# Kernel optimization log

Hardware: AMD Instinct MI355X
Metric: run time of the kernel (lower is better)

Reference implementation:

```python
import jax, jax.numpy as jnp
import numpy as np

N_NODES = 100000
N_EDGES = 1600000
K_HOPS = 10


def setup_inputs() -> dict:
    key = jax.random.key(0)
    ks = jax.random.split(key, 8)
    x = jax.random.normal(ks[0], (N_NODES, 512), dtype=jnp.float32)
    edge_src = jax.random.randint(ks[1], (N_EDGES,), 0, N_NODES, dtype=jnp.int32)
    edge_dst = jax.random.randint(ks[2], (N_EDGES,), 0, N_NODES, dtype=jnp.int32)
    # positive, roughly degree-normalized edge weights (stand-in for sym-normalized adj)
    edge_weight = jax.random.uniform(ks[3], (N_EDGES,), dtype=jnp.float32) / 16.0
    node_index = jax.random.randint(ks[4], (10000,), 0, N_NODES, dtype=jnp.int32)
    W1 = jax.random.normal(ks[5], (512, 64), dtype=jnp.float32) * 0.05
    W2 = jax.random.normal(ks[6], (64, 64), dtype=jnp.float32) * 0.05
    w_prop = jax.random.normal(ks[7], (64, 1), dtype=jnp.float32) * 0.05
    return {"x": x, "edge_src": edge_src, "edge_dst": edge_dst,
            "edge_weight": edge_weight, "node_index": node_index,
            "W1": W1, "W2": W2, "w_prop": w_prop}


def reference(x, edge_src, edge_dst, edge_weight, node_index, W1, W2, w_prop):
    # MLP (dropout is identity at inference, use_bias=False)
    h = jax.nn.relu(x @ W1)          # [N, 64]
    h = jax.nn.relu(h @ W2)          # [N, C]

    # K-hop sparse propagation: h_{k+1} = A @ h_k via edge-list SpMM
    def spmm(v):
        return jax.ops.segment_sum(edge_weight[:, None] * v[edge_src],
                                   edge_dst, num_segments=N_NODES)

    props = [h]
    cur = h
    for _ in range(K_HOPS):
        cur = spmm(cur)
        props.append(cur)
    H = jnp.stack(props, axis=1)     # [N, K+1, C]

    # sigmoid-gated combination across hops (DAGNN)
    score = jax.nn.sigmoid(H @ w_prop)        # [N, K+1, 1]
    out = jnp.sum(score * H, axis=1)          # [N, C]

    # gather requested nodes
    return out[node_index]                    # [n_idx, C]
```

## Files before the change

### kernel.cpp

```cpp
#include <hip/hip_runtime.h>
#include <hip/hip_bf16.h>

#define C 64

__device__ __forceinline__ float b2f(unsigned short s) {
    return __uint_as_float(((unsigned int)s) << 16);
}
__device__ __forceinline__ unsigned short f2b(float f) {
    unsigned int u = __float_as_uint(f);
    u = (u + 0x7FFF + ((u >> 16) & 1)) >> 16;
    return (unsigned short)u;
}

__launch_bounds__(256)
__global__ void mlp_kernel(const float* __restrict__ x,
                           const float* __restrict__ W1,
                           const float* __restrict__ W2,
                           float* __restrict__ h0,
                           unsigned short* __restrict__ hb, int nN)
{
    __shared__ float smem[5440];
    float (*As)[36] = (float(*)[36])smem;
    float (*Bs)[68] = (float(*)[68])(smem + 2304);
    float (*Hs)[68] = (float(*)[68])smem;
    float (*Ws)[68] = (float(*)[68])(smem + 4352);

    const int t  = threadIdx.x;
    const int ty = t >> 4;
    const int tx = t & 15;
    const int row0 = blockIdx.x * 64;

    float acc[4][4] = {};

    for (int k0 = 0; k0 < 512; k0 += 32) {
        #pragma unroll
        for (int h = 0; h < 2; ++h) {
            int f = t + 256 * h;
            int r  = f >> 3;
            int lk = (f & 7) * 4;
            int grow = row0 + r;
            float4 v = make_float4(0.f, 0.f, 0.f, 0.f);
            if (grow < nN) v = *(const float4*)&x[(size_t)grow * 512 + k0 + lk];
            *(float4*)&As[r][lk] = v;
        }
        #pragma unroll
        for (int h = 0; h < 2; ++h) {
            int f = t + 256 * h;
            int kr = f >> 4;
            int c4 = (f & 15) * 4;
            *(float4*)&Bs[kr][c4] = *(const float4*)&W1[(size_t)(k0 + kr) * 64 + c4];
        }
        __syncthreads();

        for (int kk = 0; kk < 32; kk += 4) {
            float4 b0 = *(float4*)&Bs[kk + 0][tx * 4];
            float4 b1 = *(float4*)&Bs[kk + 1][tx * 4];
            float4 b2 = *(float4*)&Bs[kk + 2][tx * 4];
            float4 b3 = *(float4*)&Bs[kk + 3][tx * 4];
            #pragma unroll
            for (int i = 0; i < 4; ++i) {
                float4 a = *(float4*)&As[ty * 4 + i][kk];
                acc[i][0] += a.x * b0.x + a.y * b1.x + a.z * b2.x + a.w * b3.x;
                acc[i][1] += a.x * b0.y + a.y * b1.y + a.z * b2.y + a.w * b3.y;
                acc[i][2] += a.x * b0.z + a.y * b1.z + a.z * b2.z + a.w * b3.z;
                acc[i][3] += a.x * b0.w + a.y * b1.w + a.z * b2.w + a.w * b3.w;
            }
        }
        __syncthreads();
    }

    #pragma unroll
    for (int i = 0; i < 4; ++i) {
        float4 o;
        o.x = acc[i][0] > 0.f ? acc[i][0] : 0.f;
        o.y = acc[i][1] > 0.f ? acc[i][1] : 0.f;
        o.z = acc[i][2] > 0.f ? acc[i][2] : 0.f;
        o.w = acc[i][3] > 0.f ? acc[i][3] : 0.f;
        *(float4*)&Hs[ty * 4 + i][tx * 4] = o;
    }

    float acc2[4][4] = {};
    for (int k0w = 0; k0w < 64; k0w += 16) {
        __syncthreads();
        {
            int r  = t >> 4;
            int c4 = (t & 15) * 4;
            *(float4*)&Ws[r][c4] = *(const float4*)&W2[(size_t)(k0w + r) * 64 + c4];
        }
        __syncthreads();

        for (int kk = 0; kk < 16; kk += 4) {
            float4 b0 = *(float4*)&Ws[kk + 0][tx * 4];
            float4 b1 = *(float4*)&Ws[kk + 1][tx * 4];
            float4 b2 = *(float4*)&Ws[kk + 2][tx * 4];
            float4 b3 = *(float4*)&Ws[kk + 3][tx * 4];
            #pragma unroll
            for (int i = 0; i < 4; ++i) {
                float4 a = *(float4*)&Hs[ty * 4 + i][k0w + kk];
                acc2[i][0] += a.x * b0.x + a.y * b1.x + a.z * b2.x + a.w * b3.x;
                acc2[i][1] += a.x * b0.y + a.y * b1.y + a.z * b2.y + a.w * b3.y;
                acc2[i][2] += a.x * b0.z + a.y * b1.z + a.z * b2.z + a.w * b3.z;
                acc2[i][3] += a.x * b0.w + a.y * b1.w + a.z * b2.w + a.w * b3.w;
            }
        }
    }

    #pragma unroll
    for (int i = 0; i < 4; ++i) {
        int grow = row0 + ty * 4 + i;
        if (grow < nN) {
            float4 o;
            o.x = acc2[i][0] > 0.f ? acc2[i][0] : 0.f;
            o.y = acc2[i][1] > 0.f ? acc2[i][1] : 0.f;
            o.z = acc2[i][2] > 0.f ? acc2[i][2] : 0.f;
            o.w = acc2[i][3] > 0.f ? acc2[i][3] : 0.f;
            *(float4*)&h0[(size_t)grow * 64 + tx * 4] = o;
            ushort4 ob = make_ushort4(f2b(o.x), f2b(o.y), f2b(o.z), f2b(o.w));
            *(ushort4*)&hb[(size_t)grow * 64 + tx * 4] = ob;
        }
    }
}

__launch_bounds__(256)
__global__ void count_kernel(const int* __restrict__ dst, int* __restrict__ rowptr, int nE)
{
    int e = blockIdx.x * 256 + threadIdx.x;
    if (e < nE) atomicAdd(&rowptr[dst[e]], 1);
}

__launch_bounds__(256)
__global__ void scanA(int* __restrict__ deg, int* __restrict__ bsum, int nN)
{
    __shared__ int ts[256];
    const int t = threadIdx.x;
    const int base = blockIdx.x * 1024 + t * 4;
    int v0 = 0, v1 = 0, v2 = 0, v3 = 0;
    if (base + 3 < nN) {
        int4 v = *(const int4*)&deg[base];
        v0 = v.x; v1 = v.y; v2 = v.z; v3 = v.w;
    } else {
        if (base + 0 < nN) v0 = deg[base + 0];
        if (base + 1 < nN) v1 = deg[base + 1];
        if (base + 2 < nN) v2 = deg[base + 2];
        if (base + 3 < nN) v3 = deg[base + 3];
    }
    int s = v0 + v1 + v2 + v3;
    ts[t] = s;
    __syncthreads();
    for (int d = 1; d < 256; d <<= 1) {
        int xv = (t >= d) ? ts[t - d] : 0;
        __syncthreads();
        ts[t] += xv;
        __syncthreads();
    }
    if (t == 255) bsum[blockIdx.x] = ts[255];
    int e0 = ts[t] - s;
    int e1 = e0 + v0;
    int e2 = e1 + v1;
    int e3 = e2 + v2;
    if (base + 3 < nN) {
        *(int4*)&deg[base] = make_int4(e0, e1, e2, e3);
    } else {
        if (base + 0 < nN) deg[base + 0] = e0;
        if (base + 1 < nN) deg[base + 1] = e1;
        if (base + 2 < nN) deg[base + 2] = e2;
        if (base + 3 < nN) deg[base + 3] = e3;
    }
}

__launch_bounds__(256)
__global__ void scanB(int* __restrict__ bsum, int nB)
{
    __shared__ int ts[256];
    const int t = threadIdx.x;
    int v = (t < nB) ? bsum[t] : 0;
    ts[t] = v;
    __syncthreads();
    for (int d = 1; d < 256; d <<= 1) {
        int xv = (t >= d) ? ts[t - d] : 0;
        __syncthreads();
        ts[t] += xv;
        __syncthreads();
    }
    if (t < nB) bsum[t] = ts[t] - v;
}

__launch_bounds__(256)
__global__ void scanC(int* __restrict__ deg, const int* __restrict__ bsum, int nN)
{
    const int i4 = (blockIdx.x * 256 + threadIdx.x) * 4;
    if (i4 >= nN) return;
    const int b = bsum[i4 >> 10];
    if (i4 + 3 < nN) {
        int4 v = *(int4*)&deg[i4];
        v.x += b; v.y += b; v.z += b; v.w += b;
        *(int4*)&deg[i4] = v;
    } else {
        for (int j = 0; j < 4 && i4 + j < nN; ++j) deg[i4 + j] += b;
    }
}

__launch_bounds__(256)
__global__ void fill_kernel(const int* __restrict__ src, const int* __restrict__ dst,
                            const float* __restrict__ w,
                            int* __restrict__ rowptr,
                            int2* __restrict__ cwp, int nE)
{
    int e = blockIdx.x * 256 + threadIdx.x;
    if (e >= nE) return;
    int d = dst[e];
    int pos = atomicAdd(&rowptr[d], 1);
    cwp[pos] = make_int2(src[e], __float_as_int(w[e]));
}

__launch_bounds__(256)
__global__ void spmm_fused(const int* __restrict__ rowptr,
                           const int2* __restrict__ cwp,
                           const unsigned short* __restrict__ cur,
                           unsigned short* __restrict__ nxt,
                           const int* __restrict__ idx,
                           const float* __restrict__ wp,
                           float* __restrict__ out,
                           int nN, int nI, int nodeBlocks)
{
    const int bid  = blockIdx.x;
    const int wid  = threadIdx.x >> 6;
    const int lane = threadIdx.x & 63;
    const int g = lane >> 3;
    const int q = lane & 7;

    int node, oi = -1;
    if (bid < nodeBlocks) {
        node = bid * 4 + wid;
        if (node >= nN) return;
    } else {
        oi = (bid - nodeBlocks) * 4 + wid;
        if (oi >= nI) return;
        node = idx[oi];
    }

    const int beg = (node == 0) ? 0 : rowptr[node - 1];
    const int end = rowptr[node];

    float a0[8] = {}, a1[8] = {};

    for (int e = beg; e < end; e += 16) {
        int ea = e + g;
        int eb = ea + 8;
        int2 ca = (ea < end) ? cwp[ea] : make_int2(0, 0);
        int2 cb = (eb < end) ? cwp[eb] : make_int2(0, 0);
        float wa = __int_as_float(ca.y);
        float wb = __int_as_float(cb.y);
        int4 ra = *(const int4*)&cur[(size_t)ca.x * 64 + q * 8];
        int4 rb = *(const int4*)&cur[(size_t)cb.x * 64 + q * 8];
        a0[0] += wa * __uint_as_float((unsigned)ra.x << 16);
        a0[1] += wa * __uint_as_float((unsigned)ra.x & 0xFFFF0000u);
        a0[2] += wa * __uint_as_float((unsigned)ra.y << 16);
        a0[3] += wa * __uint_as_float((unsigned)ra.y & 0xFFFF0000u);
        a0[4] += wa * __uint_as_float((unsigned)ra.z << 16);
        a0[5] += wa * __uint_as_float((unsigned)ra.z & 0xFFFF0000u);
        a0[6] += wa * __uint_as_float((unsigned)ra.w << 16);
        a0[7] += wa * __uint_as_float((unsigned)ra.w & 0xFFFF0000u);
        a1[0] += wb * __uint_as_float((unsigned)rb.x << 16);
        a1[1] += wb * __uint_as_float((unsigned)rb.x & 0xFFFF0000u);
        a1[2] += wb * __uint_as_float((unsigned)rb.y << 16);
        a1[3] += wb * __uint_as_float((unsigned)rb.y & 0xFFFF0000u);
        a1[4] += wb * __uint_as_float((unsigned)rb.z << 16);
        a1[5] += wb * __uint_as_float((unsigned)rb.z & 0xFFFF0000u);
        a1[6] += wb * __uint_as_float((unsigned)rb.w << 16);
        a1[7] += wb * __uint_as_float((unsigned)rb.w & 0xFFFF0000u);
    }
    #pragma unroll
    for (int j = 0; j < 8; ++j) a0[j] += a1[j];

    #pragma unroll
    for (int j = 0; j < 8; ++j) {
        a0[j] += __shfl_xor(a0[j], 8);
        a0[j] += __shfl_xor(a0[j], 16);
        a0[j] += __shfl_xor(a0[j], 32);
    }

    if (oi < 0) {
        if (g == 0) {
            int4 ob;
            ob.x = (int)(((unsigned)f2b(a0[1]) << 16) | (unsigned)f2b(a0[0]));
            ob.y = (int)(((unsigned)f2b(a0[3]) << 16) | (unsigned)f2b(a0[2]));
            ob.z = (int)(((unsigned)f2b(a0[5]) << 16) | (unsigned)f2b(a0[4]));
            ob.w = (int)(((unsigned)f2b(a0[7]) << 16) | (unsigned)f2b(a0[6]));
            *(int4*)&nxt[(size_t)node * 64 + q * 8] = ob;
        }
    } else {
        float s = 0.f;
        #pragma unroll
        for (int j = 0; j < 8; ++j) s += a0[j] * wp[q * 8 + j];
        s += __shfl_xor(s, 1); s += __shfl_xor(s, 2); s += __shfl_xor(s, 4);
        float gate = 1.f / (1.f + __expf(-s));
        if (g == 0) {
            float* op = &out[(size_t)oi * 64 + q * 8];
            float4 p0 = *(float4*)op;
            float4 p1 = *(float4*)(op + 4);
            p0.x += gate * a0[0]; p0.y += gate * a0[1];
            p0.z += gate * a0[2]; p0.w += gate * a0[3];
            p1.x += gate * a0[4]; p1.y += gate * a0[5];
            p1.z += gate * a0[6]; p1.w += gate * a0[7];
            *(float4*)op = p0;
            *(float4*)(op + 4) = p1;
        }
    }
}

__launch_bounds__(256)
__global__ void gate_gather(const float* __restrict__ h,
                            const int* __restrict__ idx,
                            const float* __restrict__ wp,
                            float* __restrict__ out, int nI)
{
    int gid = blockIdx.x * 256 + threadIdx.x;
    int i = gid >> 6;
    if (i >= nI) return;
    int c = gid & 63;
    int n = idx[i];
    float v = h[(size_t)n * 64 + c];
    float s = v * wp[c];
    #pragma unroll
    for (int off = 32; off > 0; off >>= 1)
        s += __shfl_xor(s, off);
    float gate = 1.f / (1.f + __expf(-s));
    out[gid] = gate * v;
}

extern "C" void kernel_launch(void* const* d_in, const int* in_sizes, int n_in,
                              void* d_out, int out_size, void* d_ws, size_t ws_size,
                              hipStream_t stream) {
    const float* x    = (const float*)d_in[0];
    const int*   esrc = (const int*)d_in[1];
    const int*   edst = (const int*)d_in[2];
    const float* ew   = (const float*)d_in[3];
    const int*   nidx = (const int*)d_in[4];
    const float* W1   = (const float*)d_in[5];
    const float* W2   = (const float*)d_in[6];
    const float* wp   = (const float*)d_in[7];
    float* out = (float*)d_out;

    const int nN = in_sizes[0] / 512;
    const int nE = in_sizes[1];
    const int nI = in_sizes[4];

    float*          h0     = (float*)d_ws;
    unsigned short* bufA   = (unsigned short*)(h0 + (size_t)nN * C);
    unsigned short* bufB   = bufA + (size_t)nN * C;
    int*            rowptr = (int*)(bufB + (size_t)nN * C);
    int2*           cwp    = (int2*)(rowptr + nN);
    int*            bsum   = (int*)bufB;

    const int nB = (nN + 1023) / 1024;

    hipMemsetAsync(rowptr, 0, (size_t)nN * sizeof(int), stream);
    count_kernel<<<(nE + 255) / 256, 256, 0, stream>>>(edst, rowptr, nE);
    scanA<<<nB, 256, 0, stream>>>(rowptr, bsum, nN);
    scanB<<<1, 256, 0, stream>>>(bsum, nB);
    scanC<<<nB, 256, 0, stream>>>(rowptr, bsum, nN);
    fill_kernel<<<(nE + 255) / 256, 256, 0, stream>>>(esrc, edst, ew, rowptr, cwp, nE);

    mlp_kernel<<<(nN + 63) / 64, 256, 0, stream>>>(x, W1, W2, h0, bufA, nN);

    gate_gather<<<(nI * 64 + 255) / 256, 256, 0, stream>>>(h0, nidx, wp, out, nI);

    unsigned short* cur = bufA;
    unsigned short* nxt = bufB;
    const int nodeBlocks = (nN + 3) / 4;
    const int idxBlocks  = (nI + 3) / 4;
    for (int k = 0; k < 10; ++k) {
        const int nb = (k == 9) ? 0 : nodeBlocks;
        spmm_fused<<<nb + idxBlocks, 256, 0, stream>>>(
            rowptr, cwp, cur, nxt, nidx, wp, out, nN, nI, nb);
        unsigned short* tmp = cur; cur = nxt; nxt = tmp;
    }
}
```

Before: 1.192 ms.

## Split bf16 hop features into two 32-channel planes and widen MLP K-tile

Stores the bf16 propagation buffers as two separate 32-channel planes and launches separate block ranges per plane. Each wavefront gathers 64-byte half-rows for 16 edges at a time. The aim is to shrink each plane's working set so the random gathers hit cache better. The cost is reading the CSR edge list twice and launching twice as many node blocks. The MLP kernel also moves to a 64-wide K tile, loads W2 once with a single barrier, and uses more shared memory.

```diff
diff --git a/kernel.cpp b/kernel.cpp
--- a/kernel.cpp
+++ b/kernel.cpp
@@ -19,9 +19,9 @@
                            float* __restrict__ h0,
                            unsigned short* __restrict__ hb, int nN)
 {
-    __shared__ float smem[5440];
-    float (*As)[36] = (float(*)[36])smem;
-    float (*Bs)[68] = (float(*)[68])(smem + 2304);
+    __shared__ float smem[8704];
+    float (*As)[68] = (float(*)[68])smem;
+    float (*Bs)[68] = (float(*)[68])(smem + 4352);
     float (*Hs)[68] = (float(*)[68])smem;
     float (*Ws)[68] = (float(*)[68])(smem + 4352);
 
@@ -30,29 +30,28 @@
     const int tx = t & 15;
     const int row0 = blockIdx.x * 64;
 
+    const int srow = t >> 4;
+    const int slk  = (t & 15) * 4;
+
     float acc[4][4] = {};
 
-    for (int k0 = 0; k0 < 512; k0 += 32) {
-        #pragma unroll
-        for (int h = 0; h < 2; ++h) {
-            int f = t + 256 * h;
-            int r  = f >> 3;
-            int lk = (f & 7) * 4;
+    for (int k0 = 0; k0 < 512; k0 += 64) {
+        #pragma unroll
+        for (int h = 0; h < 4; ++h) {
+            int r = srow + 16 * h;
             int grow = row0 + r;
             float4 v = make_float4(0.f, 0.f, 0.f, 0.f);
-            if (grow < nN) v = *(const float4*)&x[(size_t)grow * 512 + k0 + lk];
-            *(float4*)&As[r][lk] = v;
-        }
-        #pragma unroll
-        for (int h = 0; h < 2; ++h) {
-            int f = t + 256 * h;
-            int kr = f >> 4;
-            int c4 = (f & 15) * 4;
-            *(float4*)&Bs[kr][c4] = *(const float4*)&W1[(size_t)(k0 + kr) * 64 + c4];
-        }
-        __syncthreads();
-
-        for (int kk = 0; kk < 32; kk += 4) {
+            if (grow < nN) v = *(const float4*)&x[(size_t)grow * 512 + k0 + slk];
+            *(float4*)&As[r][slk] = v;
+        }
+        #pragma unroll
+        for (int h = 0; h < 4; ++h) {
+            int r = srow + 16 * h;
+            *(float4*)&Bs[r][slk] = *(const float4*)&W1[(size_t)(k0 + r) * 64 + slk];
+        }
+        __syncthreads();
+
+        for (int kk = 0; kk < 64; kk += 4) {
             float4 b0 = *(float4*)&Bs[kk + 0][tx * 4];
             float4 b1 = *(float4*)&Bs[kk + 1][tx * 4];
             float4 b2 = *(float4*)&Bs[kk + 2][tx * 4];
@@ -78,33 +77,30 @@
         o.w = acc[i][3] > 0.f ? acc[i][3] : 0.f;
         *(float4*)&Hs[ty * 4 + i][tx * 4] = o;
     }
+    #pragma unroll
+    for (int qq = 0; qq < 4; ++qq) {
+        int r = srow + 16 * qq;
+        *(float4*)&Ws[r][slk] = *(const float4*)&W2[(size_t)r * 64 + slk];
+    }
+    __syncthreads();
 
     float acc2[4][4] = {};
-    for (int k0w = 0; k0w < 64; k0w += 16) {
-        __syncthreads();
-        {
-            int r  = t >> 4;
-            int c4 = (t & 15) * 4;
-            *(float4*)&Ws[r][c4] = *(const float4*)&W2[(size_t)(k0w + r) * 64 + c4];
-        }
-        __syncthreads();
-
-        for (int kk = 0; kk < 16; kk += 4) {
-            float4 b0 = *(float4*)&Ws[kk + 0][tx * 4];
-            float4 b1 = *(float4*)&Ws[kk + 1][tx * 4];
-            float4 b2 = *(float4*)&Ws[kk + 2][tx * 4];
-            float4 b3 = *(float4*)&Ws[kk + 3][tx * 4];
-            #pragma unroll
-            for (int i = 0; i < 4; ++i) {
-                float4 a = *(float4*)&Hs[ty * 4 + i][k0w + kk];
-                acc2[i][0] += a.x * b0.x + a.y * b1.x + a.z * b2.x + a.w * b3.x;
-                acc2[i][1] += a.x * b0.y + a.y * b1.y + a.z * b2.y + a.w * b3.y;
-                acc2[i][2] += a.x * b0.z + a.y * b1.z + a.z * b2.z + a.w * b3.z;
-                acc2[i][3] += a.x * b0.w + a.y * b1.w + a.z * b2.w + a.w * b3.w;
-            }
-        }
-    }
-
+    for (int kk = 0; kk < 64; kk += 4) {
+        float4 b0 = *(float4*)&Ws[kk + 0][tx * 4];
+        float4 b1 = *(float4*)&Ws[kk + 1][tx * 4];
+        float4 b2 = *(float4*)&Ws[kk + 2][tx * 4];
+        float4 b3 = *(float4*)&Ws[kk + 3][tx * 4];
+        #pragma unroll
+        for (int i = 0; i < 4; ++i) {
+            float4 a = *(float4*)&Hs[ty * 4 + i][kk];
+            acc2[i][0] += a.x * b0.x + a.y * b1.x + a.z * b2.x + a.w * b3.x;
+            acc2[i][1] += a.x * b0.y + a.y * b1.y + a.z * b2.y + a.w * b3.y;
+            acc2[i][2] += a.x * b0.z + a.y * b1.z + a.z * b2.z + a.w * b3.z;
+            acc2[i][3] += a.x * b0.w + a.y * b1.w + a.z * b2.w + a.w * b3.w;
+        }
+    }
+
+    const size_t planeStride = (size_t)nN * 32;
     #pragma unroll
     for (int i = 0; i < 4; ++i) {
         int grow = row0 + ty * 4 + i;
@@ -116,7 +112,8 @@
             o.w = acc2[i][3] > 0.f ? acc2[i][3] : 0.f;
             *(float4*)&h0[(size_t)grow * 64 + tx * 4] = o;
             ushort4 ob = make_ushort4(f2b(o.x), f2b(o.y), f2b(o.z), f2b(o.w));
-            *(ushort4*)&hb[(size_t)grow * 64 + tx * 4] = ob;
+            *(ushort4*)&hb[(size_t)(tx >> 3) * planeStride
+                           + (size_t)grow * 32 + (tx & 7) * 4] = ob;
         }
     }
 }
@@ -226,15 +223,15 @@
     const int bid  = blockIdx.x;
     const int wid  = threadIdx.x >> 6;
     const int lane = threadIdx.x & 63;
-    const int g = lane >> 3;
-    const int q = lane & 7;
-
-    int node, oi = -1;
-    if (bid < nodeBlocks) {
-        node = bid * 4 + wid;
+    const size_t planeStride = (size_t)nN * 32;
+
+    int node, oi = -1, plane = 0;
+    if (bid < 2 * nodeBlocks) {
+        plane = (bid >= nodeBlocks) ? 1 : 0;
+        node = (bid - plane * nodeBlocks) * 4 + wid;
         if (node >= nN) return;
     } else {
-        oi = (bid - nodeBlocks) * 4 + wid;
+        oi = (bid - 2 * nodeBlocks) * 4 + wid;
         if (oi >= nI) return;
         node = idx[oi];
     }
@@ -242,54 +239,82 @@
     const int beg = (node == 0) ? 0 : rowptr[node - 1];
     const int end = rowptr[node];
 
-    float a0[8] = {}, a1[8] = {};
-
-    for (int e = beg; e < end; e += 16) {
-        int ea = e + g;
-        int eb = ea + 8;
-        int2 ca = (ea < end) ? cwp[ea] : make_int2(0, 0);
-        int2 cb = (eb < end) ? cwp[eb] : make_int2(0, 0);
-        float wa = __int_as_float(ca.y);
-        float wb = __int_as_float(cb.y);
-        int4 ra = *(const int4*)&cur[(size_t)ca.x * 64 + q * 8];
-        int4 rb = *(const int4*)&cur[(size_t)cb.x * 64 + q * 8];
-        a0[0] += wa * __uint_as_float((unsigned)ra.x << 16);
-        a0[1] += wa * __uint_as_float((unsigned)ra.x & 0xFFFF0000u);
-        a0[2] += wa * __uint_as_float((unsigned)ra.y << 16);
-        a0[3] += wa * __uint_as_float((unsigned)ra.y & 0xFFFF0000u);
-        a0[4] += wa * __uint_as_float((unsigned)ra.z << 16);
-        a0[5] += wa * __uint_as_float((unsigned)ra.z & 0xFFFF0000u);
-        a0[6] += wa * __uint_as_float((unsigned)ra.w << 16);
-        a0[7] += wa * __uint_as_float((unsigned)ra.w & 0xFFFF0000u);
-        a1[0] += wb * __uint_as_float((unsigned)rb.x << 16);
-        a1[1] += wb * __uint_as_float((unsigned)rb.x & 0xFFFF0000u);
-        a1[2] += wb * __uint_as_float((unsigned)rb.y << 16);
-        a1[3] += wb * __uint_as_float((unsigned)rb.y & 0xFFFF0000u);
-        a1[4] += wb * __uint_as_float((unsigned)rb.z << 16);
-        a1[5] += wb * __uint_as_float((unsigned)rb.z & 0xFFFF0000u);
-        a1[6] += wb * __uint_as_float((unsigned)rb.w << 16);
-        a1[7] += wb * __uint_as_float((unsigned)rb.w & 0xFFFF0000u);
-    }
-    #pragma unroll
-    for (int j = 0; j < 8; ++j) a0[j] += a1[j];
-
-    #pragma unroll
-    for (int j = 0; j < 8; ++j) {
-        a0[j] += __shfl_xor(a0[j], 8);
-        a0[j] += __shfl_xor(a0[j], 16);
-        a0[j] += __shfl_xor(a0[j], 32);
-    }
-
     if (oi < 0) {
+        const int g  = lane >> 2;
+        const int q4 = lane & 3;
+        const unsigned short* curp = cur + plane * planeStride;
+
+        float a[8] = {};
+        for (int e = beg; e < end; e += 16) {
+            int ee = e + g;
+            int2 ce = (ee < end) ? cwp[ee] : make_int2(0, 0);
+            float w = __int_as_float(ce.y);
+            int4 r = *(const int4*)&curp[(size_t)ce.x * 32 + q4 * 8];
+            a[0] += w * __uint_as_float((unsigned)r.x << 16);
+            a[1] += w * __uint_as_float((unsigned)r.x & 0xFFFF0000u);
+            a[2] += w * __uint_as_float((unsigned)r.y << 16);
+            a[3] += w * __uint_as_float((unsigned)r.y & 0xFFFF0000u);
+            a[4] += w * __uint_as_float((unsigned)r.z << 16);
+            a[5] += w * __uint_as_float((unsigned)r.z & 0xFFFF0000u);
+            a[6] += w * __uint_as_float((unsigned)r.w << 16);
+            a[7] += w * __uint_as_float((unsigned)r.w & 0xFFFF0000u);
+        }
+        #pragma unroll
+        for (int j = 0; j < 8; ++j) {
+            a[j] += __shfl_xor(a[j], 4);
+            a[j] += __shfl_xor(a[j], 8);
+            a[j] += __shfl_xor(a[j], 16);
+            a[j] += __shfl_xor(a[j], 32);
+        }
         if (g == 0) {
             int4 ob;
-            ob.x = (int)(((unsigned)f2b(a0[1]) << 16) | (unsigned)f2b(a0[0]));
-            ob.y = (int)(((unsigned)f2b(a0[3]) << 16) | (unsigned)f2b(a0[2]));
-            ob.z = (int)(((unsigned)f2b(a0[5]) << 16) | (unsigned)f2b(a0[4]));
-            ob.w = (int)(((unsigned)f2b(a0[7]) << 16) | (unsigned)f2b(a0[6]));
-            *(int4*)&nxt[(size_t)node * 64 + q * 8] = ob;
+            ob.x = (int)(((unsigned)f2b(a[1]) << 16) | (unsigned)f2b(a[0]));
+            ob.y = (int)(((unsigned)f2b(a[3]) << 16) | (unsigned)f2b(a[2]));
+            ob.z = (int)(((unsigned)f2b(a[5]) << 16) | (unsigned)f2b(a[4]));
+            ob.w = (int)(((unsigned)f2b(a[7]) << 16) | (unsigned)f2b(a[6]));
+            *(int4*)&nxt[plane * planeStride + (size_t)node * 32 + q4 * 8] = ob;
         }
     } else {
+        const int g = lane >> 3;
+        const int q = lane & 7;
+        const unsigned short* curp = cur + (q >> 2) * planeStride;
+        const int co = (q & 3) * 8;
+
+        float a0[8] = {}, a1[8] = {};
+        for (int e = beg; e < end; e += 16) {
+            int ea = e + g;
+            int eb = ea + 8;
+            int2 ca = (ea < end) ? cwp[ea] : make_int2(0, 0);
+            int2 cb = (eb < end) ? cwp[eb] : make_int2(0, 0);
+            float wa = __int_as_float(ca.y);
+            float wb = __int_as_float(cb.y);
+            int4 ra = *(const int4*)&curp[(size_t)ca.x * 32 + co];
+            int4 rb = *(const int4*)&curp[(size_t)cb.x * 32 + co];
+            a0[0] += wa * __uint_as_float((unsigned)ra.x << 16);
+            a0[1] += wa * __uint_as_float((unsigned)ra.x & 0xFFFF0000u);
+            a0[2] += wa * __uint_as_float((unsigned)ra.y << 16);
+            a0[3] += wa * __uint_as_float((unsigned)ra.y & 0xFFFF0000u);
+            a0[4] += wa * __uint_as_float((unsigned)ra.z << 16);
+            a0[5] += wa * __uint_as_float((unsigned)ra.z & 0xFFFF0000u);
+            a0[6] += wa * __uint_as_float((unsigned)ra.w << 16);
+            a0[7] += wa * __uint_as_float((unsigned)ra.w & 0xFFFF0000u);
+            a1[0] += wb * __uint_as_float((unsigned)rb.x << 16);
+            a1[1] += wb * __uint_as_float((unsigned)rb.x & 0xFFFF0000u);
+            a1[2] += wb * __uint_as_float((unsigned)rb.y << 16);
+            a1[3] += wb * __uint_as_float((unsigned)rb.y & 0xFFFF0000u);
+            a1[4] += wb * __uint_as_float((unsigned)rb.z << 16);
+            a1[5] += wb * __uint_as_float((unsigned)rb.z & 0xFFFF0000u);
+            a1[6] += wb * __uint_as_float((unsigned)rb.w << 16);
+            a1[7] += wb * __uint_as_float((unsigned)rb.w & 0xFFFF0000u);
+        }
+        #pragma unroll
+        for (int j = 0; j < 8; ++j) a0[j] += a1[j];
+        #pragma unroll
+        for (int j = 0; j < 8; ++j) {
+            a0[j] += __shfl_xor(a0[j], 8);
+            a0[j] += __shfl_xor(a0[j], 16);
+            a0[j] += __shfl_xor(a0[j], 32);
+        }
         float s = 0.f;
         #pragma unroll
         for (int j = 0; j < 8; ++j) s += a0[j] * wp[q * 8 + j];
@@ -372,7 +397,7 @@
     const int idxBlocks  = (nI + 3) / 4;
     for (int k = 0; k < 10; ++k) {
         const int nb = (k == 9) ? 0 : nodeBlocks;
-        spmm_fused<<<nb + idxBlocks, 256, 0, stream>>>(
+        spmm_fused<<<2 * nb + idxBlocks, 256, 0, stream>>>(
             rowptr, cwp, cur, nxt, nidx, wp, out, nN, nI, nb);
         unsigned short* tmp = cur; cur = nxt; nxt = tmp;
     }
```

New measurement: 1.266 ms. +6.2%, slower.
